# Performance work log

Hardware: AMD Instinct MI355X
Metric: run time of the kernel (lower is better)

Reference implementation:

```python
import jax, jax.numpy as jnp
import numpy as np
import itertools

# config: dim=256, resolution=14, key_dim=32, heads=8, attention_ratio=4, act=gelu (exact)
B, DIM, RES = 128, 256, 14
H, KD, DV = 8, 32, 128          # heads, key_dim, int(attention_ratio*key_dim)
N = RES * RES                    # 196 tokens
DH = H * DV                      # dim_head = 1024
SCALE = KD ** -0.5


def _bias_idxs():
    points = list(itertools.product(range(RES), range(RES)))
    offsets, idxs = {}, []
    for p1 in points:
        for p2 in points:
            off = (abs(p1[0] - p2[0]), abs(p1[1] - p2[1]))
            if off not in offsets:
                offsets[off] = len(offsets)
            idxs.append(offsets[off])
    return np.asarray(idxs, np.int32).reshape(N, N), len(offsets)


def _cbn(x, w, b, s, t):
    # 1x1 conv (as channel GEMM) + inference BatchNorm folded to per-channel affine
    y = jnp.einsum('bchw,co->bohw', x, w) + b[None, :, None, None]
    return y * s[None, :, None, None] + t[None, :, None, None]


def setup_inputs() -> dict:
    key = jax.random.key(0)
    ks = jax.random.split(key, 32)
    n = lambda i, sh, sc=0.05: jax.random.normal(ks[i], sh, jnp.float32) * sc
    idxs, noff = _bias_idxs()
    return {
        'hidden_states': jax.random.normal(ks[0], (B, DIM, RES, RES), jnp.float32),
        'w_q': n(1, (DIM, H * KD)), 'b_q': n(2, (H * KD,)), 's_q': 1.0 + n(3, (H * KD,)), 't_q': n(4, (H * KD,)),
        'w_k': n(5, (DIM, H * KD)), 'b_k': n(6, (H * KD,)), 's_k': 1.0 + n(7, (H * KD,)), 't_k': n(8, (H * KD,)),
        'w_v': n(9, (DIM, DH)), 'b_v': n(10, (DH,)), 's_v': 1.0 + n(11, (DH,)), 't_v': n(12, (DH,)),
        'w_vl': n(13, (DH, 1, 3, 3)), 'b_vl': n(14, (DH,)), 's_vl': 1.0 + n(15, (DH,)), 't_vl': n(16, (DH,)),
        'w_th1': n(17, (H, H), 0.2), 'b_th1': n(18, (H,)),
        'w_th2': n(19, (H, H), 0.2), 'b_th2': n(20, (H,)),
        'w_p': n(21, (DH, DIM)), 'b_p': n(22, (DIM,)), 's_p': 1.0 + n(23, (DIM,)), 't_p': n(24, (DIM,)),
        'attention_biases': n(25, (H, noff), 0.2),
        'bias_idxs': jnp.asarray(idxs),
    }


def reference(hidden_states, w_q, b_q, s_q, t_q, w_k, b_k, s_k, t_k,
              w_v, b_v, s_v, t_v, w_vl, b_vl, s_vl, t_vl,
              w_th1, b_th1, w_th2, b_th2, w_p, b_p, s_p, t_p,
              attention_biases, bias_idxs):
    b = hidden_states.shape[0]
    q = _cbn(hidden_states, w_q, b_q, s_q, t_q).reshape(b, H, KD, N).transpose(0, 1, 3, 2)  # [B,H,N,kd]
    k = _cbn(hidden_states, w_k, b_k, s_k, t_k).reshape(b, H, KD, N)                        # [B,H,kd,N]
    v_img = _cbn(hidden_states, w_v, b_v, s_v, t_v)                                          # [B,DH,res,res]
    vl = jax.lax.conv_general_dilated(v_img, w_vl, (1, 1), ((1, 1), (1, 1)),
                                      feature_group_count=DH,
                                      dimension_numbers=('NCHW', 'OIHW', 'NCHW'))
    vl = (vl + b_vl[None, :, None, None]) * s_vl[None, :, None, None] + t_vl[None, :, None, None]
    v = v_img.reshape(b, H, DV, N).transpose(0, 1, 3, 2)                                     # [B,H,N,dv]

    ab = attention_biases[:, bias_idxs]                                                      # [H,N,N]
    attn = jnp.einsum('bhnk,bhkm->bhnm', q, k) * SCALE + ab[None]                            # [B,H,N,N]
    attn = jnp.einsum('gh,bhnm->bgnm', w_th1, attn) + b_th1[None, :, None, None]             # talking head 1
    attn = jax.nn.softmax(attn, axis=-1)
    attn = jnp.einsum('gh,bhnm->bgnm', w_th2, attn) + b_th2[None, :, None, None]             # talking head 2

    out = jnp.einsum('bhnm,bhmd->bhnd', attn, v)                                             # [B,H,N,dv]
    out = out.transpose(0, 1, 3, 2).reshape(b, DH, RES, RES) + vl
    out = jax.nn.gelu(out, approximate=False)                                                # torch GELU (exact)
    return _cbn(out, w_p, b_p, s_p, t_p)                                                     # [B,dim,res,res]
```

## Files before the change

kernel.cpp:

```cpp
#include <hip/hip_runtime.h>
#include <hip/hip_bf16.h>

typedef __hip_bfloat16 bf16;
typedef __attribute__((ext_vector_type(8))) short bf16x8;
typedef __attribute__((ext_vector_type(8))) unsigned short u16x8;
typedef __attribute__((ext_vector_type(4))) float f32x4;

#define NB 128
#define CIN 256
#define NPIX 196
#define RESW 14
#define NH 8
#define KD 32
#define DV 128
#define DHID 1024
#define QKSCALE 0.17677669529663687f
#define QT 16
#define NTILE 13
#define VSTRIDE 224
#define ZPAD 232
#define XSP 264
#define GROWS 208

__device__ __forceinline__ float bf2f(unsigned short u) {
  union { unsigned int i; float f; } x; x.i = ((unsigned int)u) << 16; return x.f;
}
__device__ __forceinline__ unsigned short f2bfs(float f) {
  union { float f; unsigned int i; } u; u.f = f;
  unsigned int r = u.i + 0x7fffu + ((u.i >> 16) & 1u);
  return (unsigned short)(r >> 16);
}
__device__ __forceinline__ float gelu_exact(float x) {
  return x * 0.5f * (1.f + erff(x * 0.70710678118654752f));
}

__global__ void k_fold(
    const float* wq, const float* bq, const float* sq, const float* tq,
    const float* wk, const float* bk, const float* sk, const float* tk,
    const float* wv, const float* bv, const float* sv, const float* tv,
    const float* wvl, const float* bvl_in, const float* svl, const float* tvl,
    const float* wp, const float* bp_in, const float* sp, const float* tp,
    const float* abias, const int* bidx, const float* w1, const float* b1,
    int noff,
    short* Wt, short* Wpt, float* bcat, float* bpf, float* Wvl, float* bvlf,
    float* AB1)
{
  int i = blockIdx.x * 256 + threadIdx.x;
  if (i < 393216) {
    int o = i >> 8, c = i & 255;
    float w, s;
    if (o < 256)      { w = wq[c * 256 + o];          s = sq[o]; }
    else if (o < 512) { w = wk[c * 256 + (o - 256)];  s = sk[o - 256]; }
    else              { w = wv[c * 1024 + (o - 512)]; s = sv[o - 512]; }
    Wt[i] = (short)f2bfs(w * s);
    return;
  }
  i -= 393216;
  if (i < 1536) {
    float b, s, t;
    if (i < 256)      { b = bq[i];        s = sq[i];        t = tq[i]; }
    else if (i < 512) { b = bk[i - 256];  s = sk[i - 256];  t = tk[i - 256]; }
    else              { b = bv[i - 512];  s = sv[i - 512];  t = tv[i - 512]; }
    bcat[i] = b * s + t;
    return;
  }
  i -= 1536;
  if (i < 262144) {
    int o = i >> 10, ch = i & 1023;
    Wpt[i] = (short)f2bfs(wp[ch * 256 + o] * sp[o]);
    return;
  }
  i -= 262144;
  if (i < 256) { bpf[i] = bp_in[i] * sp[i] + tp[i]; return; }
  i -= 256;
  if (i < 9216) { int ch = i / 9; Wvl[i] = wvl[i] * svl[ch]; return; }
  i -= 9216;
  if (i < 1024) { bvlf[i] = bvl_in[i] * svl[i] + tvl[i]; return; }
  i -= 1024;
  if (i < NPIX * NPIX) {
    int idx = bidx[i];
    float a[8];
#pragma unroll
    for (int h = 0; h < 8; ++h) a[h] = abias[h * noff + idx];
#pragma unroll
    for (int g = 0; g < 8; ++g) {
      float z = b1[g];
#pragma unroll
      for (int h = 0; h < 8; ++h) z += w1[g * 8 + h] * a[h];
      AB1[(size_t)g * NPIX * NPIX + i] = z;
    }
    return;
  }
}

__global__ __launch_bounds__(512) void k_qkv(
    const float* __restrict__ X, const short* __restrict__ Wt,
    const float* __restrict__ bcat, bf16* __restrict__ Yq,
    bf16* __restrict__ Yk, bf16* __restrict__ Yv)
{
  __shared__ short Xs[112 * XSP];
  int b = blockIdx.x >> 2, half = (blockIdx.x >> 1) & 1, og = blockIdx.x & 1;
  int t = threadIdx.x;
  const float* Xb = X + (size_t)b * CIN * NPIX;

  for (int i = t; i < 256 * 28; i += 512) {
    int c = i / 28, j = i % 28;
    int ng = half * 112 + 4 * j;
    int lr = 4 * j;
    if (ng + 3 < NPIX) {
      float4 xv = *(const float4*)(Xb + c * NPIX + ng);
      Xs[(lr + 0) * XSP + c] = (short)f2bfs(xv.x);
      Xs[(lr + 1) * XSP + c] = (short)f2bfs(xv.y);
      Xs[(lr + 2) * XSP + c] = (short)f2bfs(xv.z);
      Xs[(lr + 3) * XSP + c] = (short)f2bfs(xv.w);
    } else {
#pragma unroll
      for (int e = 0; e < 4; ++e) {
        float v = (ng + e < NPIX) ? Xb[c * NPIX + ng + e] : 0.f;
        Xs[(lr + e) * XSP + c] = (short)f2bfs(v);
      }
    }
  }
  __syncthreads();

  int w = t >> 6, lane = t & 63, nl = lane & 15, grp = lane >> 4;
  int NTH = half ? 6 : 7;
  int ntb = half * 7;

  for (int mm = og * 96 + w; mm < og * 96 + 96; mm += 8) {
    if (mm < 64) {
      int ot = mm >> 1, sub = mm & 1;
      int lt0 = sub * 4;
      int ltN = sub ? (NTH - 4) : 4;
      const short* arow = Wt + (size_t)(ot * 16 + nl) * CIN;
      f32x4 acc[4];
#pragma unroll
      for (int s = 0; s < 4; ++s) acc[s] = (f32x4){0.f, 0.f, 0.f, 0.f};
#pragma unroll
      for (int kk = 0; kk < 8; ++kk) {
        bf16x8 af = *(const bf16x8*)(arow + kk * 32 + grp * 8);
#pragma unroll
        for (int s = 0; s < 4; ++s) {
          if (s < ltN) {
            bf16x8 bfr = *(const bf16x8*)(Xs + ((lt0 + s) * 16 + nl) * XSP + kk * 32 + grp * 8);
            acc[s] = __builtin_amdgcn_mfma_f32_16x16x32_bf16(af, bfr, acc[s], 0, 0, 0);
          }
        }
      }
      int o0 = ot * 16 + grp * 4;
      float4 bb = *(const float4*)(bcat + o0);
      unsigned short* dst = (unsigned short*)((o0 < 256) ? Yq : Yk);
      int ob = o0 & 255;
#pragma unroll
      for (int s = 0; s < 4; ++s) {
        if (s < ltN) {
          int n = (ntb + lt0 + s) * 16 + nl;
          if (n < NPIX) {
            ushort4 pk;
            pk.x = f2bfs(acc[s][0] + bb.x); pk.y = f2bfs(acc[s][1] + bb.y);
            pk.z = f2bfs(acc[s][2] + bb.z); pk.w = f2bfs(acc[s][3] + bb.w);
            *(ushort4*)(dst + ((size_t)b * NPIX + n) * CIN + ob) = pk;
          }
        }
      }
    } else {
      int mm2 = mm - 64;
      int cht = mm2 >> 1, sub = mm2 & 1;
      int lt0 = sub * 4;
      int ltN = sub ? (NTH - 4) : 4;
      int ch = cht * 16 + nl;
      const short* brow = Wt + (size_t)(512 + ch) * CIN;
      f32x4 acc[4];
#pragma unroll
      for (int s = 0; s < 4; ++s) acc[s] = (f32x4){0.f, 0.f, 0.f, 0.f};
#pragma unroll
      for (int kk = 0; kk < 8; ++kk) {
        bf16x8 bfr = *(const bf16x8*)(brow + kk * 32 + grp * 8);
#pragma unroll
        for (int s = 0; s < 4; ++s) {
          if (s < ltN) {
            bf16x8 af = *(const bf16x8*)(Xs + ((lt0 + s) * 16 + nl) * XSP + kk * 32 + grp * 8);
            acc[s] = __builtin_amdgcn_mfma_f32_16x16x32_bf16(af, bfr, acc[s], 0, 0, 0);
          }
        }
      }
      float bb = bcat[512 + ch];
#pragma unroll
      for (int s = 0; s < 4; ++s) {
        if (s < ltN) {
          int m0 = (ntb + lt0 + s) * 16 + grp * 4;
          if (m0 + 3 < NPIX) {
            ushort4 pk;
            pk.x = f2bfs(acc[s][0] + bb); pk.y = f2bfs(acc[s][1] + bb);
            pk.z = f2bfs(acc[s][2] + bb); pk.w = f2bfs(acc[s][3] + bb);
            *(ushort4*)((unsigned short*)Yv + ((size_t)b * DHID + ch) * VSTRIDE + m0) = pk;
          }
        }
      }
    }
  }
}

__global__ __launch_bounds__(512) void k_conv(
    const bf16* __restrict__ Yv, const float* __restrict__ Wvl,
    const float* __restrict__ bvlf, bf16* __restrict__ Gt)
{
  __shared__ short Vs[128 * ZPAD];
  int b = blockIdx.x >> 3, cg = blockIdx.x & 7;
  int t = threadIdx.x;
  const unsigned short* src = (const unsigned short*)Yv + ((size_t)b * DHID + cg * 128) * VSTRIDE;
  for (int i = t; i < 128 * 28; i += 512) {
    int ch = i / 28, j = i % 28;
    u16x8 v = *(const u16x8*)(src + ch * VSTRIDE + j * 8);
    *(u16x8*)(Vs + ch * ZPAD + j * 8) = v;
  }
  __syncthreads();

  int ch = t & 127, yg = t >> 7;
  int chg = cg * 128 + ch;
  float w9[9];
#pragma unroll
  for (int k = 0; k < 9; ++k) w9[k] = Wvl[chg * 9 + k];
  float bb = bvlf[chg];
  const short* row = Vs + ch * ZPAD;
  unsigned short* gbase = (unsigned short*)Gt + (size_t)b * GROWS * DHID + chg;

  int ylim = (yg == 3) ? 2 : 4;
  for (int yy = 0; yy < ylim; ++yy) {
    int y = yg * 4 + yy;
    float rw[3][14];
#pragma unroll
    for (int dy = 0; dy < 3; ++dy) {
      int ys = y + dy - 1;
      if (ys < 0 || ys >= RESW) {
#pragma unroll
        for (int x = 0; x < 14; ++x) rw[dy][x] = 0.f;
      } else {
#pragma unroll
        for (int x2 = 0; x2 < 7; ++x2) {
          unsigned int u = *(const unsigned int*)(row + ys * RESW + x2 * 2);
          rw[dy][x2 * 2]     = bf2f((unsigned short)(u & 0xffffu));
          rw[dy][x2 * 2 + 1] = bf2f((unsigned short)(u >> 16));
        }
      }
    }
#pragma unroll
    for (int x = 0; x < 14; ++x) {
      float a = bb;
#pragma unroll
      for (int dy = 0; dy < 3; ++dy)
#pragma unroll
        for (int dx = 0; dx < 3; ++dx) {
          int xx = x + dx - 1;
          if (xx >= 0 && xx < RESW) a += w9[dy * 3 + dx] * rw[dy][xx];
        }
      gbase[(size_t)(y * RESW + x) * DHID] = f2bfs(a);
    }
  }
}

__global__ __launch_bounds__(512) void k_attn(
    const bf16* __restrict__ Yq, const bf16* __restrict__ Yk,
    const bf16* __restrict__ Yv, const float* __restrict__ AB1,
    const float* __restrict__ w1, const float* __restrict__ w2,
    const float* __restrict__ b2, bf16* __restrict__ Gt)
{
  __shared__ short zb[NH][QT][ZPAD];
  __shared__ float red[8][NH][16];
  int id = blockIdx.x;
  int swz = (id & 7) * (NB * NTILE / 8) + (id >> 3);
  int b = swz / NTILE, tile = swz % NTILE;
  int n0 = tile * QT;
  int t = threadIdx.x;
  int w = t >> 6, lane = t & 63;
  int nl = lane & 15, grp = lane >> 4;
  int n = n0 + nl;
  int nA = (n < NPIX) ? n : (NPIX - 1);

  int t0 = w;
  int t1 = (w < 5) ? (w + 8) : ((w == 5) ? 13 : -1);

  unsigned short* gp = (unsigned short*)Gt + ((size_t)b * GROWS + nA) * DHID + w * DV;
  ushort4 cvv[8];
#pragma unroll
  for (int dt = 0; dt < 8; ++dt) cvv[dt] = *(const ushort4*)(gp + dt * 16 + grp * 4);

  const short* qrow = (const short*)Yq + ((size_t)b * NPIX + nA) * CIN;
  bf16x8 qf[8];
#pragma unroll
  for (int h = 0; h < 8; ++h) qf[h] = *(const bf16x8*)(qrow + h * 32 + grp * 8);

  const short* kbase = (const short*)Yk + (size_t)b * NPIX * CIN;
  const f32x4 NEG = (f32x4){-1e30f, -1e30f, -1e30f, -1e30f};
  f32x4 zm0[8], zm1[8];

#define DO_TILE(MT, ZM)                                                        \
  {                                                                            \
    int m0_ = (MT) * 16 + grp * 4;                                             \
    bool mv_ = (m0_ + 3) < NPIX;                                               \
    if ((MT) < 13) {                                                           \
      int mrow_ = (MT) * 16 + nl; if (mrow_ > NPIX - 1) mrow_ = NPIX - 1;      \
      const short* krow_ = kbase + (size_t)mrow_ * CIN + grp * 8;              \
      f32x4 zr_[8];                                                            \
      _Pragma("unroll")                                                        \
      for (int h = 0; h < 8; ++h) {                                            \
        bf16x8 kf_ = *(const bf16x8*)(krow_ + h * 32);                         \
        zr_[h] = __builtin_amdgcn_mfma_f32_16x16x32_bf16(                      \
            kf_, qf[h], (f32x4){0.f, 0.f, 0.f, 0.f}, 0, 0, 0);                 \
      }                                                                        \
      _Pragma("unroll")                                                        \
      for (int g = 0; g < 8; ++g) {                                            \
        if (mv_) {                                                             \
          f32x4 a_ = *(const f32x4*)(AB1 + ((size_t)g * NPIX + nA) * NPIX + m0_); \
          _Pragma("unroll")                                                    \
          for (int h = 0; h < 8; ++h) {                                        \
            float wgh_ = w1[g * 8 + h] * QKSCALE;                              \
            _Pragma("unroll")                                                  \
            for (int r = 0; r < 4; ++r) a_[r] += wgh_ * zr_[h][r];             \
          }                                                                    \
          ZM[g] = a_;                                                          \
        } else ZM[g] = NEG;                                                    \
      }                                                                        \
    } else {                                                                   \
      _Pragma("unroll")                                                        \
      for (int g = 0; g < 8; ++g) ZM[g] = NEG;                                 \
    }                                                                          \
  }

  DO_TILE(t0, zm0)
  if (t1 >= 0) { DO_TILE(t1, zm1) }
  else {
#pragma unroll
    for (int g = 0; g < 8; ++g) zm1[g] = NEG;
  }

  float mg[8];
#pragma unroll
  for (int g = 0; g < 8; ++g) {
    float m_ = fmaxf(fmaxf(zm0[g][0], zm0[g][1]), fmaxf(zm0[g][2], zm0[g][3]));
    m_ = fmaxf(m_, fmaxf(fmaxf(zm1[g][0], zm1[g][1]), fmaxf(zm1[g][2], zm1[g][3])));
    m_ = fmaxf(m_, __shfl_xor(m_, 16));
    m_ = fmaxf(m_, __shfl_xor(m_, 32));
    mg[g] = m_;
  }
  if (lane < 16) {
#pragma unroll
    for (int g = 0; g < 8; ++g) red[w][g][nl] = mg[g];
  }
  __syncthreads();
  float fmx[8];
#pragma unroll
  for (int g = 0; g < 8; ++g) {
    float m_ = red[0][g][nl];
#pragma unroll
    for (int ww = 1; ww < 8; ++ww) m_ = fmaxf(m_, red[ww][g][nl]);
    fmx[g] = m_;
  }
  float sg[8];
#pragma unroll
  for (int g = 0; g < 8; ++g) {
    float s_ = 0.f;
#pragma unroll
    for (int r = 0; r < 4; ++r) { zm0[g][r] = __expf(zm0[g][r] - fmx[g]); s_ += zm0[g][r]; }
#pragma unroll
    for (int r = 0; r < 4; ++r) { zm1[g][r] = __expf(zm1[g][r] - fmx[g]); s_ += zm1[g][r]; }
    s_ += __shfl_xor(s_, 16);
    s_ += __shfl_xor(s_, 32);
    sg[g] = s_;
  }
  __syncthreads();
  if (lane < 16) {
#pragma unroll
    for (int g = 0; g < 8; ++g) red[w][g][nl] = sg[g];
  }
  __syncthreads();
  float inv[8];
#pragma unroll
  for (int g = 0; g < 8; ++g) {
    float s_ = red[0][g][nl];
#pragma unroll
    for (int ww = 1; ww < 8; ++ww) s_ += red[ww][g][nl];
    inv[g] = 1.f / s_;
  }

  float p0[8][4], p1[8][4];
#pragma unroll
  for (int g = 0; g < 8; ++g)
#pragma unroll
    for (int r = 0; r < 4; ++r) {
      p0[g][r] = zm0[g][r] * inv[g];
      p1[g][r] = zm1[g][r] * inv[g];
    }
  int m0a = t0 * 16 + grp * 4;
  bool v0 = m0a < NPIX;
  int m0b = (t1 >= 0) ? (t1 * 16 + grp * 4) : 0;
  bool v1 = (t1 >= 0) && (m0b < NPIX);
#pragma unroll
  for (int j = 0; j < 8; ++j) {
    float b2j = b2[j];
    float a0[4] = {b2j, b2j, b2j, b2j};
    float a1[4] = {b2j, b2j, b2j, b2j};
#pragma unroll
    for (int g = 0; g < 8; ++g) {
      float wv = w2[j * 8 + g];
#pragma unroll
      for (int r = 0; r < 4; ++r) {
        a0[r] += wv * p0[g][r];
        a1[r] += wv * p1[g][r];
      }
    }
    ushort4 pk0;
    if (v0) { pk0.x = f2bfs(a0[0]); pk0.y = f2bfs(a0[1]); pk0.z = f2bfs(a0[2]); pk0.w = f2bfs(a0[3]); }
    else    { pk0.x = 0; pk0.y = 0; pk0.z = 0; pk0.w = 0; }
    *(ushort4*)&zb[j][nl][m0a] = pk0;
    if (t1 >= 0) {
      ushort4 pk1;
      if (v1) { pk1.x = f2bfs(a1[0]); pk1.y = f2bfs(a1[1]); pk1.z = f2bfs(a1[2]); pk1.w = f2bfs(a1[3]); }
      else    { pk1.x = 0; pk1.y = 0; pk1.z = 0; pk1.w = 0; }
      *(ushort4*)&zb[j][nl][m0b] = pk1;
    }
  }
  __syncthreads();

  f32x4 accO[8];
#pragma unroll
  for (int dt = 0; dt < 8; ++dt) accO[dt] = (f32x4){0.f, 0.f, 0.f, 0.f};
  const short* vbase = (const short*)Yv + ((size_t)b * DHID + w * DV) * VSTRIDE;
#pragma unroll
  for (int ks = 0; ks < 7; ++ks) {
    int moff = ks * 32 + grp * 8;
    bf16x8 Bf = *(const bf16x8*)&zb[w][nl][moff];
#pragma unroll
    for (int dt = 0; dt < 8; ++dt) {
      bf16x8 Af = *(const bf16x8*)(vbase + (size_t)(dt * 16 + nl) * VSTRIDE + moff);
      accO[dt] = __builtin_amdgcn_mfma_f32_16x16x32_bf16(Af, Bf, accO[dt], 0, 0, 0);
    }
  }

  if (n < NPIX) {
#pragma unroll
    for (int dt = 0; dt < 8; ++dt) {
      ushort4 pk;
      float pre;
      pre = accO[dt][0] + bf2f(cvv[dt].x); pk.x = f2bfs(gelu_exact(pre));
      pre = accO[dt][1] + bf2f(cvv[dt].y); pk.y = f2bfs(gelu_exact(pre));
      pre = accO[dt][2] + bf2f(cvv[dt].z); pk.z = f2bfs(gelu_exact(pre));
      pre = accO[dt][3] + bf2f(cvv[dt].w); pk.w = f2bfs(gelu_exact(pre));
      *(ushort4*)(gp + dt * 16 + grp * 4) = pk;
    }
  }
}

__global__ __launch_bounds__(256) void k_proj(
    const bf16* __restrict__ Gt, const short* __restrict__ Wpt,
    const float* __restrict__ bpf, float* __restrict__ out)
{
  int b = blockIdx.x >> 2, q = blockIdx.x & 3;
  int t = threadIdx.x, w = t >> 6, lane = t & 63, nl = lane & 15, grp = lane >> 4;
  int ot = q * 4 + w;
  const short* a0 = Wpt + (size_t)(ot * 16 + nl) * DHID + grp * 8;
  const short* bb = (const short*)Gt + (size_t)b * GROWS * DHID + (size_t)nl * DHID + grp * 8;
  f32x4 acc[13];
#pragma unroll
  for (int i = 0; i < 13; ++i) acc[i] = (f32x4){0.f, 0.f, 0.f, 0.f};
  for (int kk = 0; kk < 32; ++kk) {
    bf16x8 af = *(const bf16x8*)(a0 + kk * 32);
#pragma unroll
    for (int nt = 0; nt < 13; ++nt) {
      bf16x8 bfr = *(const bf16x8*)(bb + (size_t)(nt * 16) * DHID + kk * 32);
      acc[nt] = __builtin_amdgcn_mfma_f32_16x16x32_bf16(af, bfr, acc[nt], 0, 0, 0);
    }
  }
  int o0 = ot * 16 + grp * 4;
  float4 bv = *(const float4*)(bpf + o0);
  float ba[4] = {bv.x, bv.y, bv.z, bv.w};
#pragma unroll
  for (int nt = 0; nt < 13; ++nt) {
    int nn = nt * 16 + nl;
    if (nn < NPIX) {
#pragma unroll
      for (int r = 0; r < 4; ++r)
        out[((size_t)b * CIN + o0 + r) * NPIX + nn] = acc[nt][r] + ba[r];
    }
  }
}

extern "C" void kernel_launch(void* const* d_in, const int* in_sizes, int n_in,
                              void* d_out, int out_size, void* d_ws, size_t ws_size,
                              hipStream_t stream) {
  const float* X    = (const float*)d_in[0];
  const float* wq   = (const float*)d_in[1];
  const float* bq   = (const float*)d_in[2];
  const float* sq   = (const float*)d_in[3];
  const float* tq   = (const float*)d_in[4];
  const float* wk   = (const float*)d_in[5];
  const float* bk   = (const float*)d_in[6];
  const float* sk   = (const float*)d_in[7];
  const float* tk   = (const float*)d_in[8];
  const float* wv   = (const float*)d_in[9];
  const float* bv   = (const float*)d_in[10];
  const float* sv   = (const float*)d_in[11];
  const float* tv   = (const float*)d_in[12];
  const float* wvl  = (const float*)d_in[13];
  const float* bvl  = (const float*)d_in[14];
  const float* svl  = (const float*)d_in[15];
  const float* tvl  = (const float*)d_in[16];
  const float* w1   = (const float*)d_in[17];
  const float* b1   = (const float*)d_in[18];
  const float* w2   = (const float*)d_in[19];
  const float* b2   = (const float*)d_in[20];
  const float* wp   = (const float*)d_in[21];
  const float* bpp  = (const float*)d_in[22];
  const float* sp   = (const float*)d_in[23];
  const float* tp   = (const float*)d_in[24];
  const float* ab   = (const float*)d_in[25];
  const int*   bidx = (const int*)d_in[26];
  int noff = in_sizes[25] / NH;

  short* Wt   = (short*)d_ws;
  short* Wpt  = Wt + 393216;
  float* bcat = (float*)(Wpt + 262144);
  float* bpf  = bcat + 1536;
  float* Wvl  = bpf + 256;
  float* bvlf = Wvl + 9216;
  float* AB1  = bvlf + 1024;
  short* Yq   = (short*)(AB1 + 307328);
  short* Yk   = Yq + (size_t)NB * NPIX * CIN;
  short* Yv   = Yk + (size_t)NB * NPIX * CIN;
  short* Gt   = Yv + (size_t)NB * DHID * VSTRIDE;

  k_fold<<<2758, 256, 0, stream>>>(wq, bq, sq, tq, wk, bk, sk, tk,
                                   wv, bv, sv, tv, wvl, bvl, svl, tvl,
                                   wp, bpp, sp, tp, ab, bidx, w1, b1, noff,
                                   Wt, Wpt, bcat, bpf, Wvl, bvlf, AB1);
  k_qkv<<<NB * 4, 512, 0, stream>>>(X, Wt, bcat, (bf16*)Yq, (bf16*)Yk, (bf16*)Yv);
  k_conv<<<NB * 8, 512, 0, stream>>>((const bf16*)Yv, Wvl, bvlf, (bf16*)Gt);
  k_attn<<<NB * NTILE, 512, 0, stream>>>((const bf16*)Yq, (const bf16*)Yk,
                                         (const bf16*)Yv, AB1, w1, w2, b2, (bf16*)Gt);
  k_proj<<<NB * 4, 256, 0, stream>>>((const bf16*)Gt, Wpt, bpf, (float*)d_out);
}
```

Before: 525.2 us.

## Coarsen qkv and proj blocks, prefetch V fragments in attention, cap attn occupancy

k_qkv now uses one block per batch-half and covers all 192 output tiles, so each staged X tile in shared memory is reused by twice as many outputs. k_proj gives each wave two output tiles that share the same Gt fragment loads, which cuts B-operand traffic. In k_attn, V fragment loads are double-buffered in registers one k-step ahead, the Gt residual load moves later to shorten its register live range, and launch bounds ask for 4 blocks per CU. The price is fewer blocks for qkv and proj (256 each), which may leave CUs idle, plus higher register pressure from the doubled accumulators and prefetch buffers.

```diff
diff --git a/kernel.cpp b/kernel.cpp
--- a/kernel.cpp
+++ b/kernel.cpp
@@ -99,7 +99,7 @@
     bf16* __restrict__ Yk, bf16* __restrict__ Yv)
 {
   __shared__ short Xs[112 * XSP];
-  int b = blockIdx.x >> 2, half = (blockIdx.x >> 1) & 1, og = blockIdx.x & 1;
+  int b = blockIdx.x >> 1, half = blockIdx.x & 1;
   int t = threadIdx.x;
   const float* Xb = X + (size_t)b * CIN * NPIX;
 
@@ -127,7 +127,7 @@
   int NTH = half ? 6 : 7;
   int ntb = half * 7;
 
-  for (int mm = og * 96 + w; mm < og * 96 + 96; mm += 8) {
+  for (int mm = w; mm < 192; mm += 8) {
     if (mm < 64) {
       int ot = mm >> 1, sub = mm & 1;
       int lt0 = sub * 4;
@@ -259,7 +259,7 @@
   }
 }
 
-__global__ __launch_bounds__(512) void k_attn(
+__global__ __launch_bounds__(512, 4) void k_attn(
     const bf16* __restrict__ Yq, const bf16* __restrict__ Yk,
     const bf16* __restrict__ Yv, const float* __restrict__ AB1,
     const float* __restrict__ w1, const float* __restrict__ w2,
@@ -279,11 +279,6 @@
 
   int t0 = w;
   int t1 = (w < 5) ? (w + 8) : ((w == 5) ? 13 : -1);
-
-  unsigned short* gp = (unsigned short*)Gt + ((size_t)b * GROWS + nA) * DHID + w * DV;
-  ushort4 cvv[8];
-#pragma unroll
-  for (int dt = 0; dt < 8; ++dt) cvv[dt] = *(const ushort4*)(gp + dt * 16 + grp * 4);
 
   const short* qrow = (const short*)Yq + ((size_t)b * NPIX + nA) * CIN;
   bf16x8 qf[8];
@@ -420,21 +415,34 @@
       *(ushort4*)&zb[j][nl][m0b] = pk1;
     }
   }
+
+  unsigned short* gp = (unsigned short*)Gt + ((size_t)b * GROWS + nA) * DHID + w * DV;
+  ushort4 cvv[8];
+#pragma unroll
+  for (int dt = 0; dt < 8; ++dt) cvv[dt] = *(const ushort4*)(gp + dt * 16 + grp * 4);
   __syncthreads();
 
   f32x4 accO[8];
 #pragma unroll
   for (int dt = 0; dt < 8; ++dt) accO[dt] = (f32x4){0.f, 0.f, 0.f, 0.f};
   const short* vbase = (const short*)Yv + ((size_t)b * DHID + w * DV) * VSTRIDE;
+  bf16x8 Afq[2][8];
+#pragma unroll
+  for (int dt = 0; dt < 8; ++dt)
+    Afq[0][dt] = *(const bf16x8*)(vbase + (size_t)(dt * 16 + nl) * VSTRIDE + grp * 8);
 #pragma unroll
   for (int ks = 0; ks < 7; ++ks) {
     int moff = ks * 32 + grp * 8;
+    if (ks < 6) {
+      int mo2 = moff + 32;
+#pragma unroll
+      for (int dt = 0; dt < 8; ++dt)
+        Afq[(ks & 1) ^ 1][dt] = *(const bf16x8*)(vbase + (size_t)(dt * 16 + nl) * VSTRIDE + mo2);
+    }
     bf16x8 Bf = *(const bf16x8*)&zb[w][nl][moff];
 #pragma unroll
-    for (int dt = 0; dt < 8; ++dt) {
-      bf16x8 Af = *(const bf16x8*)(vbase + (size_t)(dt * 16 + nl) * VSTRIDE + moff);
-      accO[dt] = __builtin_amdgcn_mfma_f32_16x16x32_bf16(Af, Bf, accO[dt], 0, 0, 0);
-    }
+    for (int dt = 0; dt < 8; ++dt)
+      accO[dt] = __builtin_amdgcn_mfma_f32_16x16x32_bf16(Afq[ks & 1][dt], Bf, accO[dt], 0, 0, 0);
   }
 
   if (n < NPIX) {
@@ -455,32 +463,44 @@
     const bf16* __restrict__ Gt, const short* __restrict__ Wpt,
     const float* __restrict__ bpf, float* __restrict__ out)
 {
-  int b = blockIdx.x >> 2, q = blockIdx.x & 3;
+  int b = blockIdx.x >> 1, half = blockIdx.x & 1;
   int t = threadIdx.x, w = t >> 6, lane = t & 63, nl = lane & 15, grp = lane >> 4;
-  int ot = q * 4 + w;
-  const short* a0 = Wpt + (size_t)(ot * 16 + nl) * DHID + grp * 8;
+  int ot0 = half * 8 + w;
+  int ot1 = ot0 + 4;
+  const short* a0 = Wpt + (size_t)(ot0 * 16 + nl) * DHID + grp * 8;
+  const short* a1 = Wpt + (size_t)(ot1 * 16 + nl) * DHID + grp * 8;
   const short* bb = (const short*)Gt + (size_t)b * GROWS * DHID + (size_t)nl * DHID + grp * 8;
-  f32x4 acc[13];
-#pragma unroll
-  for (int i = 0; i < 13; ++i) acc[i] = (f32x4){0.f, 0.f, 0.f, 0.f};
+  f32x4 acc0[13], acc1[13];
+#pragma unroll
+  for (int i = 0; i < 13; ++i) {
+    acc0[i] = (f32x4){0.f, 0.f, 0.f, 0.f};
+    acc1[i] = (f32x4){0.f, 0.f, 0.f, 0.f};
+  }
   for (int kk = 0; kk < 32; ++kk) {
-    bf16x8 af = *(const bf16x8*)(a0 + kk * 32);
+    bf16x8 af0 = *(const bf16x8*)(a0 + kk * 32);
+    bf16x8 af1 = *(const bf16x8*)(a1 + kk * 32);
 #pragma unroll
     for (int nt = 0; nt < 13; ++nt) {
       bf16x8 bfr = *(const bf16x8*)(bb + (size_t)(nt * 16) * DHID + kk * 32);
-      acc[nt] = __builtin_amdgcn_mfma_f32_16x16x32_bf16(af, bfr, acc[nt], 0, 0, 0);
-    }
-  }
-  int o0 = ot * 16 + grp * 4;
-  float4 bv = *(const float4*)(bpf + o0);
-  float ba[4] = {bv.x, bv.y, bv.z, bv.w};
+      acc0[nt] = __builtin_amdgcn_mfma_f32_16x16x32_bf16(af0, bfr, acc0[nt], 0, 0, 0);
+      acc1[nt] = __builtin_amdgcn_mfma_f32_16x16x32_bf16(af1, bfr, acc1[nt], 0, 0, 0);
+    }
+  }
+  int o0 = ot0 * 16 + grp * 4;
+  int o1 = ot1 * 16 + grp * 4;
+  float4 b0 = *(const float4*)(bpf + o0);
+  float4 b1v = *(const float4*)(bpf + o1);
+  float b0a[4] = {b0.x, b0.y, b0.z, b0.w};
+  float b1a[4] = {b1v.x, b1v.y, b1v.z, b1v.w};
 #pragma unroll
   for (int nt = 0; nt < 13; ++nt) {
     int nn = nt * 16 + nl;
     if (nn < NPIX) {
 #pragma unroll
-      for (int r = 0; r < 4; ++r)
-        out[((size_t)b * CIN + o0 + r) * NPIX + nn] = acc[nt][r] + ba[r];
+      for (int r = 0; r < 4; ++r) {
+        out[((size_t)b * CIN + o0 + r) * NPIX + nn] = acc0[nt][r] + b0a[r];
+        out[((size_t)b * CIN + o1 + r) * NPIX + nn] = acc1[nt][r] + b1a[r];
+      }
     }
   }
 }
@@ -533,9 +553,9 @@
                                    wv, bv, sv, tv, wvl, bvl, svl, tvl,
                                    wp, bpp, sp, tp, ab, bidx, w1, b1, noff,
                                    Wt, Wpt, bcat, bpf, Wvl, bvlf, AB1);
-  k_qkv<<<NB * 4, 512, 0, stream>>>(X, Wt, bcat, (bf16*)Yq, (bf16*)Yk, (bf16*)Yv);
+  k_qkv<<<NB * 2, 512, 0, stream>>>(X, Wt, bcat, (bf16*)Yq, (bf16*)Yk, (bf16*)Yv);
   k_conv<<<NB * 8, 512, 0, stream>>>((const bf16*)Yv, Wvl, bvlf, (bf16*)Gt);
   k_attn<<<NB * NTILE, 512, 0, stream>>>((const bf16*)Yq, (const bf16*)Yk,
                                          (const bf16*)Yv, AB1, w1, w2, b2, (bf16*)Gt);
-  k_proj<<<NB * 4, 256, 0, stream>>>((const bf16*)Gt, Wpt, bpf, (float*)d_out);
-}
+  k_proj<<<NB * 2, 256, 0, stream>>>((const bf16*)Gt, Wpt, bpf, (float*)d_out);
+}
```

Measured after the change: 476.3 us. 1.1x faster.

## Retile QKV and projection GEMMs, defer conv load, raise attention occupancy

Applied to the files above, without the earlier changes.

k_qkv now splits each batch's pixels into four row chunks (4/3/3/3 tiles) instead of two halves times two output groups. This shrinks shared memory and has every block compute all output channels for its pixel chunk, so X is staged once per chunk. k_proj moves to 512 threads, with each block covering 8 output tiles over half the pixels, which cuts the per-wave accumulator count from 13 to 7. k_attn gains a min-blocks occupancy hint and loads the conv residual later to shorten its register live range. The occupancy hint may force register spills in the attention kernel.

```diff
diff --git a/kernel.cpp b/kernel.cpp
--- a/kernel.cpp
+++ b/kernel.cpp
@@ -98,14 +98,19 @@
     const float* __restrict__ bcat, bf16* __restrict__ Yq,
     bf16* __restrict__ Yk, bf16* __restrict__ Yv)
 {
-  __shared__ short Xs[112 * XSP];
-  int b = blockIdx.x >> 2, half = (blockIdx.x >> 1) & 1, og = blockIdx.x & 1;
+  __shared__ short Xs[64 * XSP];
+  int b = blockIdx.x >> 2, q = blockIdx.x & 3;
+  const int qs_[4] = {0, 4, 7, 10};
+  const int qc_[4] = {4, 3, 3, 3};
+  int qs = qs_[q], qc = qc_[q];
+  int rowbase = qs * 16, nrows = qc * 16;
   int t = threadIdx.x;
   const float* Xb = X + (size_t)b * CIN * NPIX;
 
-  for (int i = t; i < 256 * 28; i += 512) {
-    int c = i / 28, j = i % 28;
-    int ng = half * 112 + 4 * j;
+  int jn = nrows >> 2;
+  for (int i = t; i < 256 * jn; i += 512) {
+    int c = i / jn, j = i % jn;
+    int ng = rowbase + 4 * j;
     int lr = 4 * j;
     if (ng + 3 < NPIX) {
       float4 xv = *(const float4*)(Xb + c * NPIX + ng);
@@ -124,14 +129,10 @@
   __syncthreads();
 
   int w = t >> 6, lane = t & 63, nl = lane & 15, grp = lane >> 4;
-  int NTH = half ? 6 : 7;
-  int ntb = half * 7;
-
-  for (int mm = og * 96 + w; mm < og * 96 + 96; mm += 8) {
-    if (mm < 64) {
-      int ot = mm >> 1, sub = mm & 1;
-      int lt0 = sub * 4;
-      int ltN = sub ? (NTH - 4) : 4;
+
+  for (int mm = w; mm < 96; mm += 8) {
+    if (mm < 32) {
+      int ot = mm;
       const short* arow = Wt + (size_t)(ot * 16 + nl) * CIN;
       f32x4 acc[4];
 #pragma unroll
@@ -141,8 +142,8 @@
         bf16x8 af = *(const bf16x8*)(arow + kk * 32 + grp * 8);
 #pragma unroll
         for (int s = 0; s < 4; ++s) {
-          if (s < ltN) {
-            bf16x8 bfr = *(const bf16x8*)(Xs + ((lt0 + s) * 16 + nl) * XSP + kk * 32 + grp * 8);
+          if (s < qc) {
+            bf16x8 bfr = *(const bf16x8*)(Xs + (s * 16 + nl) * XSP + kk * 32 + grp * 8);
             acc[s] = __builtin_amdgcn_mfma_f32_16x16x32_bf16(af, bfr, acc[s], 0, 0, 0);
           }
         }
@@ -153,8 +154,8 @@
       int ob = o0 & 255;
 #pragma unroll
       for (int s = 0; s < 4; ++s) {
-        if (s < ltN) {
-          int n = (ntb + lt0 + s) * 16 + nl;
+        if (s < qc) {
+          int n = (qs + s) * 16 + nl;
           if (n < NPIX) {
             ushort4 pk;
             pk.x = f2bfs(acc[s][0] + bb.x); pk.y = f2bfs(acc[s][1] + bb.y);
@@ -164,10 +165,7 @@
         }
       }
     } else {
-      int mm2 = mm - 64;
-      int cht = mm2 >> 1, sub = mm2 & 1;
-      int lt0 = sub * 4;
-      int ltN = sub ? (NTH - 4) : 4;
+      int cht = mm - 32;
       int ch = cht * 16 + nl;
       const short* brow = Wt + (size_t)(512 + ch) * CIN;
       f32x4 acc[4];
@@ -178,8 +176,8 @@
         bf16x8 bfr = *(const bf16x8*)(brow + kk * 32 + grp * 8);
 #pragma unroll
         for (int s = 0; s < 4; ++s) {
-          if (s < ltN) {
-            bf16x8 af = *(const bf16x8*)(Xs + ((lt0 + s) * 16 + nl) * XSP + kk * 32 + grp * 8);
+          if (s < qc) {
+            bf16x8 af = *(const bf16x8*)(Xs + (s * 16 + nl) * XSP + kk * 32 + grp * 8);
             acc[s] = __builtin_amdgcn_mfma_f32_16x16x32_bf16(af, bfr, acc[s], 0, 0, 0);
           }
         }
@@ -187,8 +185,8 @@
       float bb = bcat[512 + ch];
 #pragma unroll
       for (int s = 0; s < 4; ++s) {
-        if (s < ltN) {
-          int m0 = (ntb + lt0 + s) * 16 + grp * 4;
+        if (s < qc) {
+          int m0 = (qs + s) * 16 + grp * 4;
           if (m0 + 3 < NPIX) {
             ushort4 pk;
             pk.x = f2bfs(acc[s][0] + bb); pk.y = f2bfs(acc[s][1] + bb);
@@ -259,7 +257,7 @@
   }
 }
 
-__global__ __launch_bounds__(512) void k_attn(
+__global__ __launch_bounds__(512, 4) void k_attn(
     const bf16* __restrict__ Yq, const bf16* __restrict__ Yk,
     const bf16* __restrict__ Yv, const float* __restrict__ AB1,
     const float* __restrict__ w1, const float* __restrict__ w2,
@@ -279,11 +277,6 @@
 
   int t0 = w;
   int t1 = (w < 5) ? (w + 8) : ((w == 5) ? 13 : -1);
-
-  unsigned short* gp = (unsigned short*)Gt + ((size_t)b * GROWS + nA) * DHID + w * DV;
-  ushort4 cvv[8];
-#pragma unroll
-  for (int dt = 0; dt < 8; ++dt) cvv[dt] = *(const ushort4*)(gp + dt * 16 + grp * 4);
 
   const short* qrow = (const short*)Yq + ((size_t)b * NPIX + nA) * CIN;
   bf16x8 qf[8];
@@ -420,6 +413,11 @@
       *(ushort4*)&zb[j][nl][m0b] = pk1;
     }
   }
+
+  unsigned short* gp = (unsigned short*)Gt + ((size_t)b * GROWS + nA) * DHID + w * DV;
+  ushort4 cvv[8];
+#pragma unroll
+  for (int dt = 0; dt < 8; ++dt) cvv[dt] = *(const ushort4*)(gp + dt * 16 + grp * 4);
   __syncthreads();
 
   f32x4 accO[8];
@@ -451,36 +449,43 @@
   }
 }
 
-__global__ __launch_bounds__(256) void k_proj(
+__global__ __launch_bounds__(512) void k_proj(
     const bf16* __restrict__ Gt, const short* __restrict__ Wpt,
     const float* __restrict__ bpf, float* __restrict__ out)
 {
-  int b = blockIdx.x >> 2, q = blockIdx.x & 3;
+  int b = blockIdx.x >> 2, nhalf = (blockIdx.x >> 1) & 1, og = blockIdx.x & 1;
   int t = threadIdx.x, w = t >> 6, lane = t & 63, nl = lane & 15, grp = lane >> 4;
-  int ot = q * 4 + w;
+  int ot = og * 8 + w;
+  int ntb = nhalf * 7;
+  int NTH = nhalf ? 6 : 7;
   const short* a0 = Wpt + (size_t)(ot * 16 + nl) * DHID + grp * 8;
-  const short* bb = (const short*)Gt + (size_t)b * GROWS * DHID + (size_t)nl * DHID + grp * 8;
-  f32x4 acc[13];
-#pragma unroll
-  for (int i = 0; i < 13; ++i) acc[i] = (f32x4){0.f, 0.f, 0.f, 0.f};
+  const short* bb = (const short*)Gt + (size_t)b * GROWS * DHID
+                  + (size_t)(ntb * 16 + nl) * DHID + grp * 8;
+  f32x4 acc[7];
+#pragma unroll
+  for (int i = 0; i < 7; ++i) acc[i] = (f32x4){0.f, 0.f, 0.f, 0.f};
   for (int kk = 0; kk < 32; ++kk) {
     bf16x8 af = *(const bf16x8*)(a0 + kk * 32);
 #pragma unroll
-    for (int nt = 0; nt < 13; ++nt) {
-      bf16x8 bfr = *(const bf16x8*)(bb + (size_t)(nt * 16) * DHID + kk * 32);
-      acc[nt] = __builtin_amdgcn_mfma_f32_16x16x32_bf16(af, bfr, acc[nt], 0, 0, 0);
+    for (int nt = 0; nt < 7; ++nt) {
+      if (nt < NTH) {
+        bf16x8 bfr = *(const bf16x8*)(bb + (size_t)(nt * 16) * DHID + kk * 32);
+        acc[nt] = __builtin_amdgcn_mfma_f32_16x16x32_bf16(af, bfr, acc[nt], 0, 0, 0);
+      }
     }
   }
   int o0 = ot * 16 + grp * 4;
   float4 bv = *(const float4*)(bpf + o0);
   float ba[4] = {bv.x, bv.y, bv.z, bv.w};
 #pragma unroll
-  for (int nt = 0; nt < 13; ++nt) {
-    int nn = nt * 16 + nl;
-    if (nn < NPIX) {
-#pragma unroll
-      for (int r = 0; r < 4; ++r)
-        out[((size_t)b * CIN + o0 + r) * NPIX + nn] = acc[nt][r] + ba[r];
+  for (int nt = 0; nt < 7; ++nt) {
+    if (nt < NTH) {
+      int nn = (ntb + nt) * 16 + nl;
+      if (nn < NPIX) {
+#pragma unroll
+        for (int r = 0; r < 4; ++r)
+          out[((size_t)b * CIN + o0 + r) * NPIX + nn] = acc[nt][r] + ba[r];
+      }
     }
   }
 }
@@ -537,5 +542,5 @@
   k_conv<<<NB * 8, 512, 0, stream>>>((const bf16*)Yv, Wvl, bvlf, (bf16*)Gt);
   k_attn<<<NB * NTILE, 512, 0, stream>>>((const bf16*)Yq, (const bf16*)Yk,
                                          (const bf16*)Yv, AB1, w1, w2, b2, (bf16*)Gt);
-  k_proj<<<NB * 4, 256, 0, stream>>>((const bf16*)Gt, Wpt, bpf, (float*)d_out);
-}
+  k_proj<<<NB * 4, 512, 0, stream>>>((const bf16*)Gt, Wpt, bpf, (float*)d_out);
+}
```

New measurement: 499.9 us. 4.8% less time.
